# Kernel optimization log

Measured on AMD Instinct MI355X. Metric: run time of the kernel, lower is better.

Reference implementation:

```python
import jax, jax.numpy as jnp
import numpy as np
from jax import lax

NUM_CLASSES = 10
NUM_ITERS = 3


def conv2d(x, w, b, stride):
    # x: [B,C,H,W], w: [O,I,kh,kw]
    y = lax.conv_general_dilated(x, w, (stride, stride), 'VALID',
                                 dimension_numbers=('NCHW', 'OIHW', 'NCHW'))
    return y + b[None, :, None, None]


def squash(t, axis=-1):
    sn = jnp.sum(t * t, axis=axis, keepdims=True)
    return (sn / (1.0 + sn)) * t / jnp.sqrt(sn)


def routing(x, W, num_iters=NUM_ITERS):
    # x: [B,R,Ci], W: [C,R,Ci,Co] -> outputs [B,C,Co]
    # priors[c,b,r,o] = sum_i x[b,r,i] * W[c,r,i,o]
    priors = jnp.einsum('bri,crio->cbro', x, W)  # [C,B,R,Co]
    C, B, R, Co = priors.shape
    # torch logits are [C,B,R,1,Co] but identical along Co (zeros init,
    # delta broadcast), so a [C,B,R,1] logit is mathematically identical.
    logits = jnp.zeros((C, B, R, 1), priors.dtype)
    outputs = None
    for i in range(num_iters):
        probs = jax.nn.softmax(logits, axis=2)            # over route nodes
        s = jnp.sum(probs * priors, axis=2, keepdims=True)  # [C,B,1,Co]
        outputs = squash(s, axis=-1)
        if i != num_iters - 1:
            logits = logits + jnp.sum(priors * outputs, axis=-1, keepdims=True)
    return jnp.transpose(outputs[:, :, 0, :], (1, 0, 2))  # [B,C,Co]


def setup_inputs() -> dict:
    key = jax.random.key(0)
    ks = jax.random.split(key, 16)
    B = 32
    s = 0.05
    inp = {
        'x': jax.random.normal(ks[0], (B, 1, 61, 61), jnp.float32),
        'conv0_w': jax.random.normal(ks[1], (256, 1, 9, 9), jnp.float32) * s,
        'conv0_b': jnp.zeros((256,), jnp.float32),
        'conv1_w': jax.random.normal(ks[2], (256, 256, 9, 9), jnp.float32) * s,
        'conv1_b': jnp.zeros((256,), jnp.float32),
        # 8 primary-capsule convs stacked: [8*32, 256, 9, 9]
        'prim_w': jax.random.normal(ks[3], (8 * 32, 256, 9, 9), jnp.float32) * s,
        'prim_b': jnp.zeros((8 * 32,), jnp.float32),
        'W1': jax.random.normal(ks[4], (64, 32 * 6 * 6, 8, 16), jnp.float32) * s,
        'W2': jax.random.normal(ks[5], (NUM_CLASSES, 64, 16, 16), jnp.float32) * s,
        'dec_w1': jax.random.normal(ks[6], (16 * NUM_CLASSES, 1024), jnp.float32) * s,
        'dec_b1': jnp.zeros((1024,), jnp.float32),
        'dec_w2': jax.random.normal(ks[7], (1024, 2048), jnp.float32) * s,
        'dec_b2': jnp.zeros((2048,), jnp.float32),
        'dec_w3': jax.random.normal(ks[8], (2048, 4096), jnp.float32) * s,
        'dec_b3': jnp.zeros((4096,), jnp.float32),
    }
    return inp


def reference(x, conv0_w, conv0_b, conv1_w, conv1_b, prim_w, prim_b,
              W1, W2, dec_w1, dec_b1, dec_w2, dec_b2, dec_w3, dec_b3):
    B = x.shape[0]
    h = jax.nn.relu(conv2d(x, conv0_w, conv0_b, 2))       # [B,256,27,27]
    h = jax.nn.relu(conv2d(h, conv1_w, conv1_b, 1))       # [B,256,19,19]
    # primary capsules: 8 convs of 32 channels each, k9 s2 -> [B,256,6,6]
    p = conv2d(h, prim_w, prim_b, 2)
    # torch: each capsule conv -> view(B, 32*6*6, 1), cat on last -> [B,1152,8]
    p = p.reshape(B, 8, 32 * 6 * 6)                        # [B,8,1152]
    p = jnp.transpose(p, (0, 2, 1))                        # [B,1152,8]
    p = squash(p, axis=-1)
    u = routing(p, W1)                                     # [B,64,16]
    v = routing(u, W2)                                     # [B,10,16]
    classes = jnp.sqrt(jnp.sum(v * v, axis=-1))            # [B,10]
    classes = jax.nn.softmax(classes, axis=-1)
    y = jax.nn.one_hot(jnp.argmax(classes, axis=1), NUM_CLASSES,
                       dtype=v.dtype)                       # [B,10]
    y = lax.stop_gradient(y)
    z = (v * y[:, :, None]).reshape(B, -1)                 # [B,160]
    d = jax.nn.relu(z @ dec_w1 + dec_b1)
    d = jax.nn.relu(d @ dec_w2 + dec_b2)
    reconstructions = jax.nn.sigmoid(d @ dec_w3 + dec_b3)  # [B,4096]
    return classes, reconstructions
```

## Files before the change

### kernel.cpp

```cpp
#include <hip/hip_runtime.h>
#include <hip/hip_bf16.h>
#include <math.h>


#define NB 32

typedef _Float16 f16;
typedef f16 f16x2 __attribute__((ext_vector_type(2)));
typedef f16 f16x4 __attribute__((ext_vector_type(4)));
typedef f16 f16x8 __attribute__((ext_vector_type(8)));
typedef float f32x4 __attribute__((ext_vector_type(4)));

__device__ __forceinline__ int swz(int row, int q) {
  return row * 64 + ((q * 16) ^ (((row >> 1) & 3) << 4));
}

__global__ __launch_bounds__(256) void wprep_kernel(const float* __restrict__ w,
                                                    f16* __restrict__ wo) {
  int idx = blockIdx.x * 256 + threadIdx.x;
  int oc = idx >> 8, ic = idx & 255;
  const float* src = w + (size_t)(oc * 256 + ic) * 81;
  f16* dst = wo + oc * 256 + ic;
  for (int tap = 0; tap < 81; ++tap)
    dst[(size_t)tap * 65536] = (f16)src[tap];
}

__global__ __launch_bounds__(256) void conv0_kernel(
    const float* __restrict__ x, const float* __restrict__ w,
    const float* __restrict__ bias, f16* __restrict__ outf) {
  int b = blockIdx.x, ocg = blockIdx.y, z = blockIdx.z;
  __shared__ float img[61 * 61];
  __shared__ __align__(16) float wl[81][32];
  int t = threadIdx.x;
  for (int i = t; i < 61 * 61; i += 256) img[i] = x[b * 3721 + i];
  for (int i = t; i < 81 * 32; i += 256) {
    int k = i >> 5, oc = i & 31;
    wl[k][oc] = w[(ocg * 32 + oc) * 81 + k];
  }
  __syncthreads();
  int ocs = (t & 7) * 4;
  int pg  = t >> 3;
  int oc0 = ocg * 32 + ocs;
  float b0 = bias[oc0 + 0], b1 = bias[oc0 + 1], b2 = bias[oc0 + 2],
        b3 = bias[oc0 + 3];
  for (int p = pg + z * 32; p < 729; p += 64) {
    int oh = p / 27, ow = p - oh * 27;
    float a0 = 0.f, a1 = 0.f, a2 = 0.f, a3 = 0.f;
    const float* ib = &img[oh * 2 * 61 + ow * 2];
#pragma unroll
    for (int kh = 0; kh < 9; ++kh) {
#pragma unroll
      for (int kw = 0; kw < 9; ++kw) {
        float v = ib[kh * 61 + kw];
        const float4 wv =
            *reinterpret_cast<const float4*>(&wl[kh * 9 + kw][ocs]);
        a0 += v * wv.x; a1 += v * wv.y; a2 += v * wv.z; a3 += v * wv.w;
      }
    }
    int po = oh * 28 + ow;
    f16x4 hv;
    hv[0] = (f16)fmaxf(a0 + b0, 0.f);
    hv[1] = (f16)fmaxf(a1 + b1, 0.f);
    hv[2] = (f16)fmaxf(a2 + b2, 0.f);
    hv[3] = (f16)fmaxf(a3 + b3, 0.f);
    *(f16x4*)&outf[((size_t)b * 756 + po) * 256 + oc0] = hv;
  }
}

__global__ __launch_bounds__(256, 2) void conv1_mfma(
    const f16* __restrict__ xin,
    const f16* __restrict__ wA,
    f16* __restrict__ part) {
  int b = blockIdx.x, ocg = blockIdx.y, ksp = blockIdx.z;
  __shared__ __align__(16) f16 blds[784 * 32];
  __shared__ __align__(16) f16 alds[2][64 * 32];
  int t = threadIdx.x;
  int w = t >> 6, lane = t & 63, kg = lane >> 4, ln = lane & 15;
  int aoc = t >> 2, aq = t & 3;
  int prow[6];
#pragma unroll
  for (int nf = 0; nf < 6; ++nf) {
    int n = w * 96 + nf * 16 + ln;
    int oh = n / 20, ow = n - oh * 20;
    prow[nf] = oh * 28 + ow;
  }
  f32x4 acc[4][6];
#pragma unroll
  for (int m = 0; m < 4; ++m)
#pragma unroll
    for (int nf = 0; nf < 6; ++nf) acc[m][nf] = (f32x4){0.f, 0.f, 0.f, 0.f};

  const f16* xb = xin + (size_t)b * 756 * 256 + ksp * 64;
  const f16* ab = wA + (size_t)(ocg * 64 + aoc) * 256 + ksp * 64 + aq * 8;
  for (int icc = 0; icc < 2; ++icc) {
    __syncthreads();
    for (int i = t; i < 3136; i += 256) {
      int p28 = i >> 2, q = i & 3;
      int p = (p28 < 756) ? p28 : (p28 - 28);
      f16x8 v = *(const f16x8*)(xb + (size_t)p * 256 + icc * 32 + q * 8);
      *(f16x8*)((char*)blds + swz(p28, q)) = v;
    }
    {
      f16x8 v = *(const f16x8*)(ab + icc * 32);
      *(f16x8*)((char*)alds[0] + swz(aoc, aq)) = v;
    }
    __syncthreads();
    for (int tap = 0; tap < 81; ++tap) {
      int cur = tap & 1;
      if (tap < 80) {
        f16x8 v = *(const f16x8*)(ab + (size_t)(tap + 1) * 65536 + icc * 32);
        *(f16x8*)((char*)alds[cur ^ 1] + swz(aoc, aq)) = v;
      }
      int kh = tap / 9, kw = tap - kh * 9;
      int shift = kh * 28 + kw;
      f16x8 af[4];
#pragma unroll
      for (int m = 0; m < 4; ++m)
        af[m] = *(const f16x8*)((const char*)alds[cur] + swz(m * 16 + ln, kg));
      f16x8 bf[6];
#pragma unroll
      for (int nf = 0; nf < 6; ++nf)
        bf[nf] = *(const f16x8*)((const char*)blds + swz(prow[nf] + shift, kg));
#pragma unroll
      for (int m = 0; m < 4; ++m)
#pragma unroll
        for (int nf = 0; nf < 6; ++nf)
          acc[m][nf] = __builtin_amdgcn_mfma_f32_16x16x32_f16(
              af[m], bf[nf], acc[m][nf], 0, 0, 0);
      __syncthreads();
    }
  }
  f16* pout = part + ((size_t)ksp * 32 + b) * 384 * 256 + ocg * 64;
#pragma unroll
  for (int m = 0; m < 4; ++m)
#pragma unroll
    for (int nf = 0; nf < 6; ++nf) {
      int n = w * 96 + nf * 16 + ln;
      int oc = m * 16 + kg * 4;
      f16x4 v;
#pragma unroll
      for (int j = 0; j < 4; ++j) v[j] = (f16)acc[m][nf][j];
      *(f16x4*)(pout + (size_t)n * 256 + oc) = v;
    }
}

__global__ void comb1_kernel(const f16* __restrict__ part,
                             const float* __restrict__ bias,
                             f16* __restrict__ h1f) {
  int idx = blockIdx.x * 256 + threadIdx.x;
  if (idx >= 32 * 380 * 32) return;
  int ocq = idx & 31, rem = idx >> 5;
  int p = rem % 380, b = rem / 380;
  float a[8];
#pragma unroll
  for (int j = 0; j < 8; ++j) a[j] = bias[ocq * 8 + j];
#pragma unroll
  for (int k = 0; k < 4; ++k) {
    f16x8 v = *(const f16x8*)&part[(((size_t)k * 32 + b) * 384 + p) * 256 +
                                   ocq * 8];
#pragma unroll
    for (int j = 0; j < 8; ++j) a[j] += (float)v[j];
  }
  f16x8 o;
#pragma unroll
  for (int j = 0; j < 8; ++j) o[j] = (f16)fmaxf(a[j], 0.f);
  *(f16x8*)&h1f[((size_t)b * 380 + p) * 256 + ocq * 8] = o;
}

__global__ __launch_bounds__(256, 2) void prim_mfma(
    const f16* __restrict__ xin,
    const f16* __restrict__ wB,
    float* __restrict__ part2) {
  int ip = blockIdx.x, ocg = blockIdx.y, ksp = blockIdx.z;
  __shared__ __align__(16) f16 blds[768 * 32];
  __shared__ __align__(16) f16 alds[2][128 * 32];
  int t = threadIdx.x;
  int w = t >> 6, lane = t & 63, kg = lane >> 4, ln = lane & 15;
  int mg = w >> 1, ng = w & 1;
  int rbase[3];
#pragma unroll
  for (int nf = 0; nf < 3; ++nf) {
    int rem = nf * 16 + ln;
    int oh6 = rem >> 3, ow6 = rem & 7;
    rbase[nf] = ng * 384 + oh6 * 40 + ow6 * 2;
  }
  f32x4 acc[4][3];
#pragma unroll
  for (int m = 0; m < 4; ++m)
#pragma unroll
    for (int nf = 0; nf < 3; ++nf) acc[m][nf] = (f32x4){0.f, 0.f, 0.f, 0.f};

  for (int i = t; i < 3072; i += 256) {
    int pos = i >> 2, q = i & 3;
    int img = pos >= 384 ? 1 : 0;
    int p = pos - img * 384;
    if (p >= 380) p -= 20;
    f16x8 v = *(const f16x8*)(xin +
        ((size_t)(ip * 2 + img) * 380 + p) * 256 + ksp * 32 + q * 8);
    *(f16x8*)((char*)blds + swz(pos, q)) = v;
  }
  const f16* ab = wB + (size_t)(ocg * 128) * 256 + ksp * 32;
#pragma unroll
  for (int i = t; i < 512; i += 256) {
    int oc = i >> 2, q = i & 3;
    f16x8 v = *(const f16x8*)(ab + (size_t)oc * 256 + q * 8);
    *(f16x8*)((char*)alds[0] + swz(oc, q)) = v;
  }
  __syncthreads();
  for (int tap = 0; tap < 81; ++tap) {
    int cur = tap & 1;
    if (tap < 80) {
#pragma unroll
      for (int i = t; i < 512; i += 256) {
        int oc = i >> 2, q = i & 3;
        f16x8 v = *(const f16x8*)(ab + (size_t)(tap + 1) * 65536 +
                                  (size_t)oc * 256 + q * 8);
        *(f16x8*)((char*)alds[cur ^ 1] + swz(oc, q)) = v;
      }
    }
    int kh = tap / 9, kw = tap - kh * 9;
    int shift = kh * 20 + kw;
    f16x8 af[4];
#pragma unroll
    for (int m = 0; m < 4; ++m)
      af[m] = *(const f16x8*)((const char*)alds[cur] +
                              swz((mg * 4 + m) * 16 + ln, kg));
    f16x8 bf[3];
#pragma unroll
    for (int nf = 0; nf < 3; ++nf)
      bf[nf] = *(const f16x8*)((const char*)blds + swz(rbase[nf] + shift, kg));
#pragma unroll
    for (int m = 0; m < 4; ++m)
#pragma unroll
      for (int nf = 0; nf < 3; ++nf)
        acc[m][nf] = __builtin_amdgcn_mfma_f32_16x16x32_f16(
            af[m], bf[nf], acc[m][nf], 0, 0, 0);
    __syncthreads();
  }
  float* pout = part2 + ((size_t)ksp * 16 + ip) * 96 * 256 + ocg * 128;
#pragma unroll
  for (int m = 0; m < 4; ++m)
#pragma unroll
    for (int nf = 0; nf < 3; ++nf) {
      int n = ng * 48 + nf * 16 + ln;
      int oc = (mg * 4 + m) * 16 + kg * 4;
      *(f32x4*)(pout + (size_t)n * 256 + oc) = acc[m][nf];
    }
}

__global__ void comb2_kernel(const float* __restrict__ part2,
                             float* __restrict__ sum2) {
  int idx = blockIdx.x * 256 + threadIdx.x;
  if (idx >= 16 * 96 * 256) return;
  float a = 0.f;
#pragma unroll
  for (int k = 0; k < 8; ++k) a += part2[(size_t)k * 393216 + idx];
  sum2[idx] = a;
}

__global__ void prim_squash_kernel(const float* __restrict__ sum2,
                                   const float* __restrict__ bias,
                                   float* __restrict__ caps) {
  int idx = blockIdx.x * blockDim.x + threadIdx.x;
  if (idx >= NB * 1152) return;
  int b = idx / 1152, r = idx - b * 1152;
  int m = r / 36, s = r - m * 36;
  int oh6 = s / 6, ow6 = s - oh6 * 6;
  int n = (b & 1) * 48 + oh6 * 8 + ow6;
  const float* src = sum2 + ((size_t)(b >> 1) * 96 + n) * 256;
  float tv[8];
  float sn = 0.f;
#pragma unroll
  for (int g = 0; g < 8; ++g) {
    float v = src[g * 32 + m] + bias[g * 32 + m];
    tv[g] = v;
    sn += v * v;
  }
  float sc = sqrtf(sn) / (1.f + sn);
#pragma unroll
  for (int g = 0; g < 8; ++g) caps[idx * 8 + g] = tv[g] * sc;
}

__global__ __launch_bounds__(256) void priors1_kernel(
    const float* __restrict__ x,
    const float* __restrict__ W,
    f16* __restrict__ pri) {
  int c = blockIdx.x, rt = blockIdx.y;
  int r0 = rt * 32;
  __shared__ __align__(16) float xl[32 * 32 * 8];
  int t = threadIdx.x;
  for (int q = t; q < 2048; q += 256) {
    int b = q >> 6, j = q & 63;
    *(float4*)&xl[b * 256 + j * 4] =
        *(const float4*)&x[(size_t)b * 9216 + r0 * 8 + j * 4];
  }
  int rl = t >> 3, oq = t & 7;
  float w0[8], w1[8];
#pragma unroll
  for (int i = 0; i < 8; ++i) {
    const float2 wv = *(const float2*)&W[
        (((size_t)c * 1152 + r0 + rl) * 8 + i) * 16 + 2 * oq];
    w0[i] = wv.x; w1[i] = wv.y;
  }
  __syncthreads();
  f16* pout = pri + (size_t)c * 32 * 18432 + (r0 + rl) * 16 + 2 * oq;
#pragma unroll 4
  for (int b = 0; b < 32; ++b) {
    const float4 x0 = *(const float4*)&xl[b * 256 + rl * 8];
    const float4 x1 = *(const float4*)&xl[b * 256 + rl * 8 + 4];
    float s0 = x0.x * w0[0] + x0.y * w0[1] + x0.z * w0[2] + x0.w * w0[3] +
               x1.x * w0[4] + x1.y * w0[5] + x1.z * w0[6] + x1.w * w0[7];
    float s1 = x0.x * w1[0] + x0.y * w1[1] + x0.z * w1[2] + x0.w * w1[3] +
               x1.x * w1[4] + x1.y * w1[5] + x1.z * w1[6] + x1.w * w1[7];
    f16x2 hv; hv[0] = (f16)s0; hv[1] = (f16)s1;
    *(f16x2*)(pout + (size_t)b * 18432) = hv;
  }
}

__global__ __launch_bounds__(512) void route1_kernel(
    const f16* __restrict__ pri,
    float* __restrict__ out) {
  constexpr int R = 1152;
  constexpr int NREG = 36;
  int c = blockIdx.x, b = blockIdx.y;
  __shared__ float lg[R], pr[R];
  __shared__ float redA[8], redB[8];
  __shared__ float sred[8][16];
  __shared__ float vsh[17];
  int t    = threadIdx.x;
  int o    = t & 15;
  int rhi  = t >> 4;
  int wid  = t >> 6;
  int lane = t & 63;
  const f16* pb = pri + ((size_t)c * 32 + b) * (R * 16);

  float prireg[NREG];
#pragma unroll
  for (int k = 0; k < NREG; ++k)
    prireg[k] = (float)pb[(k * 32 + rhi) * 16 + o];
  for (int r = t; r < R; r += 512) lg[r] = 0.f;
  __syncthreads();

  for (int it = 0; it < 3; ++it) {
    float lm = -1e30f;
    for (int r = t; r < R; r += 512) lm = fmaxf(lm, lg[r]);
#pragma unroll
    for (int s2 = 1; s2 <= 32; s2 <<= 1) lm = fmaxf(lm, __shfl_xor(lm, s2));
    if (lane == 0) redA[wid] = lm;
    __syncthreads();
    if (t == 0) {
      float m8 = redA[0];
#pragma unroll
      for (int w = 1; w < 8; ++w) m8 = fmaxf(m8, redA[w]);
      redA[0] = m8;
    }
    __syncthreads();
    float m = redA[0];
    float ls = 0.f;
    for (int r = t; r < R; r += 512) {
      float e = __expf(lg[r] - m);
      pr[r] = e;
      ls += e;
    }
#pragma unroll
    for (int s2 = 1; s2 <= 32; s2 <<= 1) ls += __shfl_xor(ls, s2);
    if (lane == 0) redB[wid] = ls;
    __syncthreads();
    if (t == 0) {
      float s8 = 0.f;
#pragma unroll
      for (int w = 0; w < 8; ++w) s8 += redB[w];
      redB[0] = s8;
    }
    __syncthreads();
    float denom = redB[0];
    float part = 0.f;
#pragma unroll
    for (int k = 0; k < NREG; ++k) part += pr[k * 32 + rhi] * prireg[k];
    part += __shfl_xor(part, 16);
    part += __shfl_xor(part, 32);
    if (lane < 16) sred[wid][lane] = part;
    __syncthreads();
    if (t < 16) {
      float sv = 0.f;
#pragma unroll
      for (int w = 0; w < 8; ++w) sv += sred[w][t];
      vsh[t] = sv / denom;
    }
    __syncthreads();
    if (t == 0) {
      float sn = 0.f;
#pragma unroll
      for (int oo = 0; oo < 16; ++oo) sn += vsh[oo] * vsh[oo];
      vsh[16] = sqrtf(sn) / (1.f + sn);
    }
    __syncthreads();
    if (it < 2) {
      float vo = vsh[o] * vsh[16];
#pragma unroll
      for (int k = 0; k < NREG; ++k) {
        float val = prireg[k] * vo;
        val += __shfl_xor(val, 1);
        val += __shfl_xor(val, 2);
        val += __shfl_xor(val, 4);
        val += __shfl_xor(val, 8);
        if (o == 0) lg[k * 32 + rhi] += val;
      }
      __syncthreads();
    }
  }
  if (t < 16) out[((size_t)b * 64 + c) * 16 + t] = vsh[t] * vsh[16];
}

template <int R, int CI>
__global__ __launch_bounds__(512) void routing_kernel(
    const float* __restrict__ x,
    const float* __restrict__ W,
    float* __restrict__ out) {
  constexpr int NREG = R * 16 / 512;
  int c = blockIdx.x, b = blockIdx.y;
  int C = gridDim.x;
  __shared__ float xls[R * CI];
  extern __shared__ float rdyn[];
  float* lg = rdyn;
  float* pr = rdyn + R;
  __shared__ float redA[8], redB[8];
  __shared__ float sred[8][16];
  __shared__ float vsh[17];
  int t    = threadIdx.x;
  int o    = t & 15;
  int rhi  = t >> 4;
  int wid  = t >> 6;
  int lane = t & 63;
  const float* xb = x + (size_t)b * R * CI;
  const float* Wc = W + (size_t)c * R * CI * 16;

  for (int i = t; i < R * CI; i += 512) xls[i] = xb[i];
  for (int r = t; r < R; r += 512) lg[r] = 0.f;
  __syncthreads();

  float pri[NREG];
#pragma unroll
  for (int k = 0; k < NREG; ++k) {
    int r = k * 32 + rhi;
    float s = 0.f;
#pragma unroll
    for (int i = 0; i < CI; ++i)
      s += xls[r * CI + i] * Wc[((size_t)r * CI + i) * 16 + o];
    pri[k] = s;
  }

  for (int it = 0; it < 3; ++it) {
    float lm = -1e30f;
    for (int r = t; r < R; r += 512) lm = fmaxf(lm, lg[r]);
#pragma unroll
    for (int s2 = 1; s2 <= 32; s2 <<= 1) lm = fmaxf(lm, __shfl_xor(lm, s2));
    if (lane == 0) redA[wid] = lm;
    __syncthreads();
    if (t == 0) {
      float m8 = redA[0];
#pragma unroll
      for (int w = 1; w < 8; ++w) m8 = fmaxf(m8, redA[w]);
      redA[0] = m8;
    }
    __syncthreads();
    float m = redA[0];
    float ls = 0.f;
    for (int r = t; r < R; r += 512) {
      float e = __expf(lg[r] - m);
      pr[r] = e;
      ls += e;
    }
#pragma unroll
    for (int s2 = 1; s2 <= 32; s2 <<= 1) ls += __shfl_xor(ls, s2);
    if (lane == 0) redB[wid] = ls;
    __syncthreads();
    if (t == 0) {
      float s8 = 0.f;
#pragma unroll
      for (int w = 0; w < 8; ++w) s8 += redB[w];
      redB[0] = s8;
    }
    __syncthreads();
    float denom = redB[0];
    float part = 0.f;
#pragma unroll
    for (int k = 0; k < NREG; ++k) part += pr[k * 32 + rhi] * pri[k];
    part += __shfl_xor(part, 16);
    part += __shfl_xor(part, 32);
    if (lane < 16) sred[wid][lane] = part;
    __syncthreads();
    if (t < 16) {
      float sv = 0.f;
#pragma unroll
      for (int w = 0; w < 8; ++w) sv += sred[w][t];
      vsh[t] = sv / denom;
    }
    __syncthreads();
    if (t == 0) {
      float sn = 0.f;
#pragma unroll
      for (int oo = 0; oo < 16; ++oo) sn += vsh[oo] * vsh[oo];
      vsh[16] = sqrtf(sn) / (1.f + sn);
    }
    __syncthreads();
    if (it < 2) {
      float vo = vsh[o] * vsh[16];
#pragma unroll
      for (int k = 0; k < NREG; ++k) {
        float val = pri[k] * vo;
        val += __shfl_xor(val, 1);
        val += __shfl_xor(val, 2);
        val += __shfl_xor(val, 4);
        val += __shfl_xor(val, 8);
        if (o == 0) lg[k * 32 + rhi] += val;
      }
      __syncthreads();
    }
  }
  if (t < 16) out[((size_t)b * C + c) * 16 + t] = vsh[t] * vsh[16];
}

__global__ void classes_kernel(const float* __restrict__ v,
                               float* __restrict__ outc,
                               int* __restrict__ amaxb) {
  int b = blockIdx.x;
  int t = threadIdx.x;
  __shared__ float nrm[10];
  if (t < 10) {
    float sn = 0.f;
#pragma unroll
    for (int o = 0; o < 16; ++o) {
      float xv = v[(b * 10 + t) * 16 + o];
      sn += xv * xv;
    }
    nrm[t] = sqrtf(sn);
  }
  __syncthreads();
  if (t == 0) {
    float m = nrm[0];
    int am = 0;
    for (int c = 1; c < 10; ++c)
      if (nrm[c] > m) { m = nrm[c]; am = c; }
    float s = 0.f;
    float e[10];
    for (int c = 0; c < 10; ++c) { e[c] = __expf(nrm[c] - m); s += e[c]; }
    for (int c = 0; c < 10; ++c) outc[b * 10 + c] = e[c] / s;
    amaxb[b] = am;
  }
}

__global__ __launch_bounds__(256) void fc1s_kernel(
    const float* __restrict__ v, const int* __restrict__ amaxb,
    const float* __restrict__ w, const float* __restrict__ bias,
    float* __restrict__ out) {
  int n  = blockIdx.x * 256 + threadIdx.x;
  int b0 = blockIdx.y * 8;
  __shared__ float vls[8][16];
  __shared__ int ams[8];
  int t = threadIdx.x;
  if (t < 8) ams[t] = amaxb[b0 + t];
  __syncthreads();
  if (t < 128) {
    int bb = t >> 4, oo = t & 15;
    vls[bb][oo] = v[((b0 + bb) * 10 + ams[bb]) * 16 + oo];
  }
  __syncthreads();
  float bv = bias[n];
#pragma unroll
  for (int bb = 0; bb < 8; ++bb) {
    int row0 = ams[bb] * 16;
    float acc = bv;
#pragma unroll
    for (int oo = 0; oo < 16; ++oo)
      acc += vls[bb][oo] * w[(size_t)(row0 + oo) * 1024 + n];
    out[(size_t)(b0 + bb) * 1024 + n] = fmaxf(acc, 0.f);
  }
}

template <int K, int KCH>
__global__ __launch_bounds__(256) void fcsplit_kernel(
    const float* __restrict__ in, const float* __restrict__ w,
    float* __restrict__ pbuf, int N) {
  int n  = blockIdx.x * 256 + threadIdx.x;
  int b0 = blockIdx.y * 8;
  int k0 = blockIdx.z * KCH;
  __shared__ __align__(16) float inl[KCH * 8];
  for (int idx = threadIdx.x; idx < 8 * KCH; idx += 256) {
    int bb = idx / KCH, k = idx - bb * KCH;
    inl[k * 8 + bb] = in[(size_t)(b0 + bb) * K + k0 + k];
  }
  __syncthreads();
  float acc[8];
#pragma unroll
  for (int bb = 0; bb < 8; ++bb) acc[bb] = 0.f;
  for (int k = 0; k < KCH; ++k) {
    float wv = w[(size_t)(k0 + k) * N + n];
    const float4 i0 = *reinterpret_cast<const float4*>(&inl[k * 8]);
    const float4 i1 = *reinterpret_cast<const float4*>(&inl[k * 8 + 4]);
    acc[0] += i0.x * wv; acc[1] += i0.y * wv;
    acc[2] += i0.z * wv; acc[3] += i0.w * wv;
    acc[4] += i1.x * wv; acc[5] += i1.y * wv;
    acc[6] += i1.z * wv; acc[7] += i1.w * wv;
  }
#pragma unroll
  for (int bb = 0; bb < 8; ++bb)
    pbuf[((size_t)blockIdx.z * 32 + b0 + bb) * N + n] = acc[bb];
}

template <int KS, bool RELU, bool SIG>
__global__ void fccomb_kernel(const float* __restrict__ pbuf,
                              const float* __restrict__ bias,
                              float* __restrict__ out, int N) {
  int idx = blockIdx.x * 256 + threadIdx.x;
  if (idx >= 32 * N) return;
  int b = idx / N, n = idx - b * N;
  float a = bias[n];
#pragma unroll
  for (int kz = 0; kz < KS; ++kz) a += pbuf[((size_t)kz * 32 + b) * N + n];
  if (RELU) a = fmaxf(a, 0.f);
  if (SIG)  a = 1.f / (1.f + __expf(-a));
  out[idx] = a;
}

extern "C" void kernel_launch(void* const* d_in, const int* in_sizes, int n_in,
                              void* d_out, int out_size, void* d_ws,
                              size_t ws_size, hipStream_t stream) {
  const float* x       = (const float*)d_in[0];
  const float* conv0_w = (const float*)d_in[1];
  const float* conv0_b = (const float*)d_in[2];
  const float* conv1_w = (const float*)d_in[3];
  const float* conv1_b = (const float*)d_in[4];
  const float* prim_w  = (const float*)d_in[5];
  const float* prim_b  = (const float*)d_in[6];
  const float* W1      = (const float*)d_in[7];
  const float* W2      = (const float*)d_in[8];
  const float* dec_w1  = (const float*)d_in[9];
  const float* dec_b1  = (const float*)d_in[10];
  const float* dec_w2  = (const float*)d_in[11];
  const float* dec_b2  = (const float*)d_in[12];
  const float* dec_w3  = (const float*)d_in[13];
  const float* dec_b3  = (const float*)d_in[14];
  float* out = (float*)d_out;

  float* ws    = (float*)d_ws;
  float* caps  = ws;
  float* u     = caps + 294912;
  float* vc    = u + 32768;
  int*   amaxb = (int*)(vc + 5120);
  float* trans = vc + 5120 + 32;

  f16* wA    = (f16*)trans;
  f16* wB    = wA + 5308416;
  f16* h0f   = wB + 5308416;
  f16* h1f   = h0f + 6193152;
  f16* part1 = h1f + 3112960;
  float* part2 = (float*)part1;
  float* sum2  = part2 + 3145728;
  f16* pri1  = (f16*)trans;
  float* d1  = trans;
  float* d2  = d1 + 32768;
  float* pb2 = d2 + 65536;
  float* pb3 = pb2 + 262144;

  wprep_kernel<<<256, 256, 0, stream>>>(conv1_w, wA);
  wprep_kernel<<<256, 256, 0, stream>>>(prim_w, wB);

  conv0_kernel<<<dim3(NB, 8, 2), 256, 0, stream>>>(x, conv0_w, conv0_b, h0f);

  conv1_mfma<<<dim3(NB, 4, 4), 256, 0, stream>>>(h0f, wA, part1);
  comb1_kernel<<<1520, 256, 0, stream>>>(part1, conv1_b, h1f);

  prim_mfma<<<dim3(16, 2, 8), 256, 0, stream>>>(h1f, wB, part2);
  comb2_kernel<<<1536, 256, 0, stream>>>(part2, sum2);

  prim_squash_kernel<<<(NB * 1152 + 255) / 256, 256, 0, stream>>>(sum2, prim_b,
                                                                  caps);

  priors1_kernel<<<dim3(64, 36), 256, 0, stream>>>(caps, W1, pri1);
  route1_kernel<<<dim3(64, NB), 512, 0, stream>>>(pri1, u);

  routing_kernel<64, 16>
      <<<dim3(10, NB), 512, 2 * 64 * sizeof(float), stream>>>(u, W2, vc);

  classes_kernel<<<NB, 64, 0, stream>>>(vc, out, amaxb);

  fc1s_kernel<<<dim3(4, 4), 256, 0, stream>>>(vc, amaxb, dec_w1, dec_b1, d1);

  fcsplit_kernel<1024, 256>
      <<<dim3(8, 4, 4), 256, 0, stream>>>(d1, dec_w2, pb2, 2048);
  fccomb_kernel<4, true, false>
      <<<256, 256, 0, stream>>>(pb2, dec_b2, d2, 2048);

  fcsplit_kernel<2048, 256>
      <<<dim3(16, 4, 8), 256, 0, stream>>>(d2, dec_w3, pb3, 4096);
  fccomb_kernel<8, false, true>
      <<<512, 256, 0, stream>>>(pb3, dec_b3, out + 320, 4096);
}
```

Measured before the change: 459.5 us.

## Unroll conv1 tap loop by two with quad-buffered weights and coalesce wprep

The conv1 MFMA loop now processes two filter taps per iteration using four LDS weight slots, halving the number of block barriers and prefetching two taps ahead. The input LDS tile shrinks by dropping the padded rows, and invalid output columns are clamped to row zero. The weight-prep transpose stages each output channel's weights through LDS so global reads are coalesced. The last prefetch reads one tap past the weight array, and the smaller LDS tile relies on out-of-range reads only feeding discarded outputs.

```diff
diff --git a/kernel.cpp b/kernel.cpp
--- a/kernel.cpp
+++ b/kernel.cpp
@@ -17,12 +17,17 @@
 
 __global__ __launch_bounds__(256) void wprep_kernel(const float* __restrict__ w,
                                                     f16* __restrict__ wo) {
-  int idx = blockIdx.x * 256 + threadIdx.x;
-  int oc = idx >> 8, ic = idx & 255;
-  const float* src = w + (size_t)(oc * 256 + ic) * 81;
-  f16* dst = wo + oc * 256 + ic;
+  __shared__ f16 tile[256][82];
+  int t = threadIdx.x;
+  const float* src = w + (size_t)blockIdx.x * 20736;
+  for (int j = t; j < 20736; j += 256) {
+    int r = j / 81, c = j - r * 81;
+    tile[r][c] = (f16)src[j];
+  }
+  __syncthreads();
+  f16* dst = wo + blockIdx.x * 256 + t;
   for (int tap = 0; tap < 81; ++tap)
-    dst[(size_t)tap * 65536] = (f16)src[tap];
+    dst[(size_t)tap * 65536] = tile[t][tap];
 }
 
 __global__ __launch_bounds__(256) void conv0_kernel(
@@ -72,8 +77,8 @@
     const f16* __restrict__ wA,
     f16* __restrict__ part) {
   int b = blockIdx.x, ocg = blockIdx.y, ksp = blockIdx.z;
-  __shared__ __align__(16) f16 blds[784 * 32];
-  __shared__ __align__(16) f16 alds[2][64 * 32];
+  __shared__ __align__(16) f16 blds[756 * 32];
+  __shared__ __align__(16) f16 alds[4][64 * 32];
   int t = threadIdx.x;
   int w = t >> 6, lane = t & 63, kg = lane >> 4, ln = lane & 15;
   int aoc = t >> 2, aq = t & 3;
@@ -82,7 +87,7 @@
   for (int nf = 0; nf < 6; ++nf) {
     int n = w * 96 + nf * 16 + ln;
     int oh = n / 20, ow = n - oh * 20;
-    prow[nf] = oh * 28 + ow;
+    prow[nf] = (n < 380 && ow < 19) ? (oh * 28 + ow) : 0;
   }
   f32x4 acc[4][6];
 #pragma unroll
@@ -94,29 +99,56 @@
   const f16* ab = wA + (size_t)(ocg * 64 + aoc) * 256 + ksp * 64 + aq * 8;
   for (int icc = 0; icc < 2; ++icc) {
     __syncthreads();
-    for (int i = t; i < 3136; i += 256) {
-      int p28 = i >> 2, q = i & 3;
-      int p = (p28 < 756) ? p28 : (p28 - 28);
+    for (int i = t; i < 3024; i += 256) {
+      int p = i >> 2, q = i & 3;
       f16x8 v = *(const f16x8*)(xb + (size_t)p * 256 + icc * 32 + q * 8);
-      *(f16x8*)((char*)blds + swz(p28, q)) = v;
+      *(f16x8*)((char*)blds + swz(p, q)) = v;
     }
     {
-      f16x8 v = *(const f16x8*)(ab + icc * 32);
-      *(f16x8*)((char*)alds[0] + swz(aoc, aq)) = v;
-    }
-    __syncthreads();
-    for (int tap = 0; tap < 81; ++tap) {
-      int cur = tap & 1;
-      if (tap < 80) {
-        f16x8 v = *(const f16x8*)(ab + (size_t)(tap + 1) * 65536 + icc * 32);
-        *(f16x8*)((char*)alds[cur ^ 1] + swz(aoc, aq)) = v;
+      f16x8 v0 = *(const f16x8*)(ab + icc * 32);
+      *(f16x8*)((char*)alds[0] + swz(aoc, aq)) = v0;
+      f16x8 v1 = *(const f16x8*)(ab + 65536 + icc * 32);
+      *(f16x8*)((char*)alds[1] + swz(aoc, aq)) = v1;
+    }
+    __syncthreads();
+    for (int g = 0; g < 40; ++g) {
+      int cur = g & 1;
+      {
+        f16x8 v0 = *(const f16x8*)(ab + (size_t)(2 * g + 2) * 65536 + icc * 32);
+        *(f16x8*)((char*)alds[(cur ^ 1) * 2] + swz(aoc, aq)) = v0;
+        f16x8 v1 = *(const f16x8*)(ab + (size_t)(2 * g + 3) * 65536 + icc * 32);
+        *(f16x8*)((char*)alds[(cur ^ 1) * 2 + 1] + swz(aoc, aq)) = v1;
       }
-      int kh = tap / 9, kw = tap - kh * 9;
-      int shift = kh * 28 + kw;
+#pragma unroll
+      for (int sub = 0; sub < 2; ++sub) {
+        int tap = 2 * g + sub;
+        int kh = tap / 9, kw = tap - kh * 9;
+        int shift = kh * 28 + kw;
+        const char* ap = (const char*)alds[cur * 2 + sub];
+        f16x8 af[4];
+#pragma unroll
+        for (int m = 0; m < 4; ++m)
+          af[m] = *(const f16x8*)(ap + swz(m * 16 + ln, kg));
+        f16x8 bf[6];
+#pragma unroll
+        for (int nf = 0; nf < 6; ++nf)
+          bf[nf] =
+              *(const f16x8*)((const char*)blds + swz(prow[nf] + shift, kg));
+#pragma unroll
+        for (int m = 0; m < 4; ++m)
+#pragma unroll
+          for (int nf = 0; nf < 6; ++nf)
+            acc[m][nf] = __builtin_amdgcn_mfma_f32_16x16x32_f16(
+                af[m], bf[nf], acc[m][nf], 0, 0, 0);
+      }
+      __syncthreads();
+    }
+    {
+      int shift = 8 * 28 + 8;
       f16x8 af[4];
 #pragma unroll
       for (int m = 0; m < 4; ++m)
-        af[m] = *(const f16x8*)((const char*)alds[cur] + swz(m * 16 + ln, kg));
+        af[m] = *(const f16x8*)((const char*)alds[0] + swz(m * 16 + ln, kg));
       f16x8 bf[6];
 #pragma unroll
       for (int nf = 0; nf < 6; ++nf)
@@ -127,7 +159,6 @@
         for (int nf = 0; nf < 6; ++nf)
           acc[m][nf] = __builtin_amdgcn_mfma_f32_16x16x32_f16(
               af[m], bf[nf], acc[m][nf], 0, 0, 0);
-      __syncthreads();
     }
   }
   f16* pout = part + ((size_t)ksp * 32 + b) * 384 * 256 + ocg * 64;
```

New measurement: 461.4 us. About the same (+0.4%).

## Split conv grids finer, fuse prim reduce with squash, transpose weights via LDS

Applied to the files above, without the earlier changes.

conv1 now splits each image's output positions into two halves, which doubles the block count and shrinks LDS and accumulator use so three blocks can share a CU. prim_mfma processes one image per block instead of two and holds fewer M tiles per wave, again to give more blocks and occupancy. The split-K reduction is fused with the primary-capsule squash, which drops the sum2 buffer and one launch. Both weight-prep passes are merged into one kernel that stages each row in shared memory so global reads are coalesced. The cost is more redundant loading of activations and weights per block, since each weight tile is now fetched by twice as many blocks.

```diff
diff --git a/kernel.cpp b/kernel.cpp
--- a/kernel.cpp
+++ b/kernel.cpp
@@ -15,14 +15,29 @@
   return row * 64 + ((q * 16) ^ (((row >> 1) & 3) << 4));
 }
 
-__global__ __launch_bounds__(256) void wprep_kernel(const float* __restrict__ w,
-                                                    f16* __restrict__ wo) {
-  int idx = blockIdx.x * 256 + threadIdx.x;
-  int oc = idx >> 8, ic = idx & 255;
-  const float* src = w + (size_t)(oc * 256 + ic) * 81;
-  f16* dst = wo + oc * 256 + ic;
+__global__ __launch_bounds__(256) void wprep_kernel(
+    const float* __restrict__ w1, const float* __restrict__ w2,
+    f16* __restrict__ wo1, f16* __restrict__ wo2) {
+  __shared__ f16 tile[256][82];
+  int bi = blockIdx.x;
+  const float* src;
+  f16* dst;
+  if (bi < 256) {
+    src = w1 + (size_t)bi * 20736;
+    dst = wo1 + bi * 256;
+  } else {
+    src = w2 + (size_t)(bi - 256) * 20736;
+    dst = wo2 + (bi - 256) * 256;
+  }
+  int t = threadIdx.x;
+  for (int j = t; j < 20736; j += 256) {
+    int r = j / 81, c = j - r * 81;
+    tile[r][c] = (f16)src[j];
+  }
+  __syncthreads();
+  f16* d = dst + t;
   for (int tap = 0; tap < 81; ++tap)
-    dst[(size_t)tap * 65536] = (f16)src[tap];
+    d[(size_t)tap * 65536] = tile[t][tap];
 }
 
 __global__ __launch_bounds__(256) void conv0_kernel(
@@ -67,38 +82,42 @@
   }
 }
 
-__global__ __launch_bounds__(256, 2) void conv1_mfma(
+__global__ __launch_bounds__(256, 3) void conv1_mfma(
     const f16* __restrict__ xin,
     const f16* __restrict__ wA,
     f16* __restrict__ part) {
-  int b = blockIdx.x, ocg = blockIdx.y, ksp = blockIdx.z;
-  __shared__ __align__(16) f16 blds[784 * 32];
+  int b = blockIdx.x, ocg = blockIdx.y;
+  int ksp = blockIdx.z >> 1, ph = blockIdx.z & 1;
+  __shared__ __align__(16) f16 blds[504 * 32];
   __shared__ __align__(16) f16 alds[2][64 * 32];
   int t = threadIdx.x;
   int w = t >> 6, lane = t & 63, kg = lane >> 4, ln = lane & 15;
   int aoc = t >> 2, aq = t & 3;
-  int prow[6];
-#pragma unroll
-  for (int nf = 0; nf < 6; ++nf) {
-    int n = w * 96 + nf * 16 + ln;
+  int row0 = ph * 252;
+  int prow[3];
+#pragma unroll
+  for (int nf = 0; nf < 3; ++nf) {
+    int n = ph * 192 + w * 48 + nf * 16 + ln;
     int oh = n / 20, ow = n - oh * 20;
-    prow[nf] = oh * 28 + ow;
-  }
-  f32x4 acc[4][6];
+    if (oh > 18) oh = 18;
+    if (ow > 18) ow = 18;
+    prow[nf] = oh * 28 + ow - row0;
+  }
+  f32x4 acc[4][3];
 #pragma unroll
   for (int m = 0; m < 4; ++m)
 #pragma unroll
-    for (int nf = 0; nf < 6; ++nf) acc[m][nf] = (f32x4){0.f, 0.f, 0.f, 0.f};
+    for (int nf = 0; nf < 3; ++nf) acc[m][nf] = (f32x4){0.f, 0.f, 0.f, 0.f};
 
   const f16* xb = xin + (size_t)b * 756 * 256 + ksp * 64;
   const f16* ab = wA + (size_t)(ocg * 64 + aoc) * 256 + ksp * 64 + aq * 8;
   for (int icc = 0; icc < 2; ++icc) {
     __syncthreads();
-    for (int i = t; i < 3136; i += 256) {
-      int p28 = i >> 2, q = i & 3;
-      int p = (p28 < 756) ? p28 : (p28 - 28);
-      f16x8 v = *(const f16x8*)(xb + (size_t)p * 256 + icc * 32 + q * 8);
-      *(f16x8*)((char*)blds + swz(p28, q)) = v;
+    for (int i = t; i < 2016; i += 256) {
+      int p = i >> 2, q = i & 3;
+      f16x8 v =
+          *(const f16x8*)(xb + (size_t)(row0 + p) * 256 + icc * 32 + q * 8);
+      *(f16x8*)((char*)blds + swz(p, q)) = v;
     }
     {
       f16x8 v = *(const f16x8*)(ab + icc * 32);
@@ -117,14 +136,15 @@
 #pragma unroll
       for (int m = 0; m < 4; ++m)
         af[m] = *(const f16x8*)((const char*)alds[cur] + swz(m * 16 + ln, kg));
-      f16x8 bf[6];
-#pragma unroll
-      for (int nf = 0; nf < 6; ++nf)
-        bf[nf] = *(const f16x8*)((const char*)blds + swz(prow[nf] + shift, kg));
+      f16x8 bf[3];
+#pragma unroll
+      for (int nf = 0; nf < 3; ++nf)
+        bf[nf] =
+            *(const f16x8*)((const char*)blds + swz(prow[nf] + shift, kg));
 #pragma unroll
       for (int m = 0; m < 4; ++m)
 #pragma unroll
-        for (int nf = 0; nf < 6; ++nf)
+        for (int nf = 0; nf < 3; ++nf)
           acc[m][nf] = __builtin_amdgcn_mfma_f32_16x16x32_f16(
               af[m], bf[nf], acc[m][nf], 0, 0, 0);
       __syncthreads();
@@ -134,8 +154,8 @@
 #pragma unroll
   for (int m = 0; m < 4; ++m)
 #pragma unroll
-    for (int nf = 0; nf < 6; ++nf) {
-      int n = w * 96 + nf * 16 + ln;
+    for (int nf = 0; nf < 3; ++nf) {
+      int n = ph * 192 + w * 48 + nf * 16 + ln;
       int oc = m * 16 + kg * 4;
       f16x4 v;
 #pragma unroll
@@ -167,40 +187,36 @@
   *(f16x8*)&h1f[((size_t)b * 380 + p) * 256 + ocq * 8] = o;
 }
 
-__global__ __launch_bounds__(256, 2) void prim_mfma(
+__global__ __launch_bounds__(256, 3) void prim_mfma(
     const f16* __restrict__ xin,
     const f16* __restrict__ wB,
     float* __restrict__ part2) {
-  int ip = blockIdx.x, ocg = blockIdx.y, ksp = blockIdx.z;
-  __shared__ __align__(16) f16 blds[768 * 32];
+  int b = blockIdx.x, ocg = blockIdx.y, ksp = blockIdx.z;
+  __shared__ __align__(16) f16 blds[384 * 32];
   __shared__ __align__(16) f16 alds[2][128 * 32];
   int t = threadIdx.x;
   int w = t >> 6, lane = t & 63, kg = lane >> 4, ln = lane & 15;
-  int mg = w >> 1, ng = w & 1;
   int rbase[3];
 #pragma unroll
   for (int nf = 0; nf < 3; ++nf) {
     int rem = nf * 16 + ln;
     int oh6 = rem >> 3, ow6 = rem & 7;
-    rbase[nf] = ng * 384 + oh6 * 40 + ow6 * 2;
-  }
-  f32x4 acc[4][3];
-#pragma unroll
-  for (int m = 0; m < 4; ++m)
+    rbase[nf] = oh6 * 40 + ow6 * 2;
+  }
+  f32x4 acc[2][3];
+#pragma unroll
+  for (int m = 0; m < 2; ++m)
 #pragma unroll
     for (int nf = 0; nf < 3; ++nf) acc[m][nf] = (f32x4){0.f, 0.f, 0.f, 0.f};
 
-  for (int i = t; i < 3072; i += 256) {
+  for (int i = t; i < 1536; i += 256) {
     int pos = i >> 2, q = i & 3;
-    int img = pos >= 384 ? 1 : 0;
-    int p = pos - img * 384;
-    if (p >= 380) p -= 20;
-    f16x8 v = *(const f16x8*)(xin +
-        ((size_t)(ip * 2 + img) * 380 + p) * 256 + ksp * 32 + q * 8);
+    int p = pos < 380 ? pos : pos - 20;
+    f16x8 v = *(const f16x8*)(xin + ((size_t)b * 380 + p) * 256 + ksp * 32 +
+                              q * 8);
     *(f16x8*)((char*)blds + swz(pos, q)) = v;
   }
   const f16* ab = wB + (size_t)(ocg * 128) * 256 + ksp * 32;
-#pragma unroll
   for (int i = t; i < 512; i += 256) {
     int oc = i >> 2, q = i & 3;
     f16x8 v = *(const f16x8*)(ab + (size_t)oc * 256 + q * 8);
@@ -210,7 +226,6 @@
   for (int tap = 0; tap < 81; ++tap) {
     int cur = tap & 1;
     if (tap < 80) {
-#pragma unroll
       for (int i = t; i < 512; i += 256) {
         int oc = i >> 2, q = i & 3;
         f16x8 v = *(const f16x8*)(ab + (size_t)(tap + 1) * 65536 +
@@ -220,65 +235,65 @@
     }
     int kh = tap / 9, kw = tap - kh * 9;
     int shift = kh * 20 + kw;
-    f16x8 af[4];
-#pragma unroll
-    for (int m = 0; m < 4; ++m)
+    f16x8 af[2];
+#pragma unroll
+    for (int m = 0; m < 2; ++m)
       af[m] = *(const f16x8*)((const char*)alds[cur] +
-                              swz((mg * 4 + m) * 16 + ln, kg));
+                              swz((w * 2 + m) * 16 + ln, kg));
     f16x8 bf[3];
 #pragma unroll
     for (int nf = 0; nf < 3; ++nf)
       bf[nf] = *(const f16x8*)((const char*)blds + swz(rbase[nf] + shift, kg));
 #pragma unroll
-    for (int m = 0; m < 4; ++m)
+    for (int m = 0; m < 2; ++m)
 #pragma unroll
       for (int nf = 0; nf < 3; ++nf)
         acc[m][nf] = __builtin_amdgcn_mfma_f32_16x16x32_f16(
             af[m], bf[nf], acc[m][nf], 0, 0, 0);
     __syncthreads();
   }
-  float* pout = part2 + ((size_t)ksp * 16 + ip) * 96 * 256 + ocg * 128;
-#pragma unroll
-  for (int m = 0; m < 4; ++m)
+  float* pout = part2 + ((size_t)ksp * 32 + b) * 48 * 256 + ocg * 128;
+#pragma unroll
+  for (int m = 0; m < 2; ++m)
 #pragma unroll
     for (int nf = 0; nf < 3; ++nf) {
-      int n = ng * 48 + nf * 16 + ln;
-      int oc = (mg * 4 + m) * 16 + kg * 4;
+      int n = nf * 16 + ln;
+      int oc = (w * 2 + m) * 16 + kg * 4;
       *(f32x4*)(pout + (size_t)n * 256 + oc) = acc[m][nf];
     }
 }
 
-__global__ void comb2_kernel(const float* __restrict__ part2,
-                             float* __restrict__ sum2) {
-  int idx = blockIdx.x * 256 + threadIdx.x;
-  if (idx >= 16 * 96 * 256) return;
+__global__ __launch_bounds__(256) void combsq_kernel(
+    const float* __restrict__ part2,
+    const float* __restrict__ bias, float* __restrict__ caps) {
+  int bn = blockIdx.x;
+  int b = bn / 48, n = bn - b * 48;
+  int ow6 = n & 7;
+  if (ow6 >= 6) return;
+  int oh6 = n >> 3, s = oh6 * 6 + ow6;
+  __shared__ float al[256];
+  int oc = threadIdx.x;
   float a = 0.f;
 #pragma unroll
-  for (int k = 0; k < 8; ++k) a += part2[(size_t)k * 393216 + idx];
-  sum2[idx] = a;
-}
-
-__global__ void prim_squash_kernel(const float* __restrict__ sum2,
-                                   const float* __restrict__ bias,
-                                   float* __restrict__ caps) {
-  int idx = blockIdx.x * blockDim.x + threadIdx.x;
-  if (idx >= NB * 1152) return;
-  int b = idx / 1152, r = idx - b * 1152;
-  int m = r / 36, s = r - m * 36;
-  int oh6 = s / 6, ow6 = s - oh6 * 6;
-  int n = (b & 1) * 48 + oh6 * 8 + ow6;
-  const float* src = sum2 + ((size_t)(b >> 1) * 96 + n) * 256;
-  float tv[8];
-  float sn = 0.f;
-#pragma unroll
-  for (int g = 0; g < 8; ++g) {
-    float v = src[g * 32 + m] + bias[g * 32 + m];
-    tv[g] = v;
-    sn += v * v;
-  }
-  float sc = sqrtf(sn) / (1.f + sn);
-#pragma unroll
-  for (int g = 0; g < 8; ++g) caps[idx * 8 + g] = tv[g] * sc;
+  for (int k = 0; k < 8; ++k)
+    a += part2[(((size_t)k * 32 + b) * 48 + n) * 256 + oc];
+  al[oc] = a;
+  __syncthreads();
+  if (oc < 32) {
+    int m = oc;
+    float tv[8];
+    float sn = 0.f;
+#pragma unroll
+    for (int g = 0; g < 8; ++g) {
+      float v = al[g * 32 + m] + bias[g * 32 + m];
+      tv[g] = v;
+      sn += v * v;
+    }
+    float sc = sqrtf(sn) / (1.f + sn);
+#pragma unroll
+    for (int g = 0; g < 8; ++g)
+      caps[((size_t)b * 1152 + m * 36 + s) * 8 + g] = tv[g] * sc;
+  }
 }
 
 __global__ __launch_bounds__(256) void priors1_kernel(
@@ -656,26 +671,21 @@
   f16* h1f   = h0f + 6193152;
   f16* part1 = h1f + 3112960;
   float* part2 = (float*)part1;
-  float* sum2  = part2 + 3145728;
   f16* pri1  = (f16*)trans;
   float* d1  = trans;
   float* d2  = d1 + 32768;
   float* pb2 = d2 + 65536;
   float* pb3 = pb2 + 262144;
 
-  wprep_kernel<<<256, 256, 0, stream>>>(conv1_w, wA);
-  wprep_kernel<<<256, 256, 0, stream>>>(prim_w, wB);
+  wprep_kernel<<<512, 256, 0, stream>>>(conv1_w, prim_w, wA, wB);
 
   conv0_kernel<<<dim3(NB, 8, 2), 256, 0, stream>>>(x, conv0_w, conv0_b, h0f);
 
-  conv1_mfma<<<dim3(NB, 4, 4), 256, 0, stream>>>(h0f, wA, part1);
+  conv1_mfma<<<dim3(NB, 4, 8), 256, 0, stream>>>(h0f, wA, part1);
   comb1_kernel<<<1520, 256, 0, stream>>>(part1, conv1_b, h1f);
 
-  prim_mfma<<<dim3(16, 2, 8), 256, 0, stream>>>(h1f, wB, part2);
-  comb2_kernel<<<1536, 256, 0, stream>>>(part2, sum2);
-
-  prim_squash_kernel<<<(NB * 1152 + 255) / 256, 256, 0, stream>>>(sum2, prim_b,
-                                                                  caps);
+  prim_mfma<<<dim3(NB, 2, 8), 256, 0, stream>>>(h1f, wB, part2);
+  combsq_kernel<<<NB * 48, 256, 0, stream>>>(part2, prim_b, caps);
 
   priors1_kernel<<<dim3(64, 36), 256, 0, stream>>>(caps, W1, pri1);
   route1_kernel<<<dim3(64, NB), 512, 0, stream>>>(pri1, u);
```

Measured after the change: 445.2 us. -3.1%, faster.
